# Kernel tuning notes

Hardware: AMD Instinct MI355X
Metric: run time of the kernel (lower is better)

The kernel has to match this reference:

```python
import jax, jax.numpy as jnp
import numpy as np

BS, D = 8192, 1024


def setup_inputs() -> dict:
    key = jax.random.key(0)
    k1, k2, k3, k4 = jax.random.split(key, 4)
    return {
        "z": jax.random.normal(k1, (BS, D), dtype=jnp.float32),
        "w": jax.random.normal(k2, (BS, D), dtype=jnp.float32),
        "u": jax.random.normal(k3, (BS, D), dtype=jnp.float32),
        "b": jax.random.normal(k4, (BS,), dtype=jnp.float32),
    }


def reference(z, w, u, b):
    # --- get_batch_corrected_u ---
    wu = jnp.sum(w * u, axis=1)                      # [bs]
    m = -1.0 + jax.nn.softplus(wu)                   # [bs]
    # NOTE: original divides by sqrt of GLOBAL sum over all of w (no axis)
    w_norm = jnp.sqrt(jnp.sum(w ** 2))               # scalar
    u_hat = u + ((m - wu)[:, None] * w) / w_norm     # [bs, d]

    # --- forward transform: diag(tanh(wTz+b)) @ u  ==  tanh(...)[:,None]*u ---
    inner = jnp.sum(w * z, axis=1) + b               # [bs]
    z_new = z + jnp.tanh(inner)[:, None] * u_hat     # [bs, d]

    # --- det_jcb evaluated with UPDATED z (as in the original code) ---
    inner2 = jnp.sum(w * z_new, axis=1) + b          # [bs]
    h_prime = 1.0 - jnp.tanh(inner2) ** 2            # [bs]
    psi_dot_u = h_prime * jnp.sum(u_hat * w, axis=1) # [bs]
    log_det = jnp.log(jnp.abs(1.0 + psi_dot_u))      # [bs]
    return z_new, log_det
```

## Files before the change

kernel.cpp:

```cpp
#include <hip/hip_runtime.h>
#include <math.h>

#define BS   8192
#define D    1024
#define TPB  256
#define NBLK 512
#define RPB  16
#define RPWV 4
#define F4R  4

typedef float floatx4 __attribute__((ext_vector_type(4)));
typedef unsigned long long u64;

__global__ __launch_bounds__(TPB, 2) void planar_persistent(
    const float* __restrict__ z, const float* __restrict__ w,
    const float* __restrict__ u, const float* __restrict__ b,
    float* __restrict__ zout, float* __restrict__ ldout,
    u64* __restrict__ slots, unsigned int* __restrict__ epoch)
{
    const int t    = threadIdx.x;
    const int wv   = t >> 6;
    const int l    = t & 63;
    const int row0 = blockIdx.x * RPB + wv * RPWV;

    __shared__ unsigned int s_e;
    __shared__ float sw[4], sg[4];
    if (t == 0)
        s_e = __hip_atomic_load(epoch, __ATOMIC_RELAXED,
                                __HIP_MEMORY_SCOPE_AGENT);

    float4 wr[RPWV][F4R];
    float  w2_s[RPWV];
    float  w2acc = 0.f;
#pragma unroll
    for (int r = 0; r < RPWV; ++r) {
        const float4* w4 = (const float4*)w + (size_t)(row0 + r) * (D / 4);
        float w2 = 0.f;
#pragma unroll
        for (int k = 0; k < F4R; ++k) {
            const float4 a = w4[l + (k << 6)];
            wr[r][k] = a;
            w2 += a.x*a.x + a.y*a.y + a.z*a.z + a.w*a.w;
        }
#pragma unroll
        for (int off = 32; off > 0; off >>= 1) w2 += __shfl_xor(w2, off, 64);
        w2_s[r] = w2;
        w2acc  += w2;
    }
    if (l == 0) sw[wv] = w2acc;
    __syncthreads();
    const unsigned int e1 = s_e + 1u;
    if (t == 0) {
        const float p = sw[0] + sw[1] + sw[2] + sw[3];
        const u64 word = ((u64)e1 << 32) | (u64)__float_as_uint(p);
        __hip_atomic_store(&slots[blockIdx.x], word, __ATOMIC_RELAXED,
                           __HIP_MEMORY_SCOPE_AGENT);
    }

    float4 vr[RPWV][F4R];
    float  wu_s[RPWV], in_s[RPWV], th_s[RPWV];
#pragma unroll
    for (int r = 0; r < RPWV; ++r) {
        const int row = row0 + r;
        const float4* z4 = (const float4*)z + (size_t)row * (D / 4);
        const float4* u4 = (const float4*)u + (size_t)row * (D / 4);
        float4 zv[F4R], uv[F4R];
#pragma unroll
        for (int k = 0; k < F4R; ++k) {
            zv[k] = z4[l + (k << 6)];
            uv[k] = u4[l + (k << 6)];
        }
        float wu = 0.f, wz = 0.f;
#pragma unroll
        for (int k = 0; k < F4R; ++k) {
            const float4 a = wr[r][k];
            wu += a.x*uv[k].x + a.y*uv[k].y + a.z*uv[k].z + a.w*uv[k].w;
            wz += a.x*zv[k].x + a.y*zv[k].y + a.z*zv[k].z + a.w*zv[k].w;
        }
#pragma unroll
        for (int off = 32; off > 0; off >>= 1) {
            wu += __shfl_xor(wu, off, 64);
            wz += __shfl_xor(wz, off, 64);
        }
        const float inner = wz + b[row];
        const float tnh   = tanhf(inner);
#pragma unroll
        for (int k = 0; k < F4R; ++k) {
            vr[r][k].x = fmaf(tnh, uv[k].x, zv[k].x);
            vr[r][k].y = fmaf(tnh, uv[k].y, zv[k].y);
            vr[r][k].z = fmaf(tnh, uv[k].z, zv[k].z);
            vr[r][k].w = fmaf(tnh, uv[k].w, zv[k].w);
        }
        wu_s[r] = wu; in_s[r] = inner; th_s[r] = tnh;
    }

    u64 a0, a1;
    for (;;) {
        a0 = __hip_atomic_load(&slots[t], __ATOMIC_RELAXED,
                               __HIP_MEMORY_SCOPE_AGENT);
        a1 = __hip_atomic_load(&slots[t + TPB], __ATOMIC_RELAXED,
                               __HIP_MEMORY_SCOPE_AGENT);
        if ((unsigned int)(a0 >> 32) == e1 &&
            (unsigned int)(a1 >> 32) == e1) break;
        __builtin_amdgcn_s_sleep(4);
    }
    float gs = __uint_as_float((unsigned int)a0)
             + __uint_as_float((unsigned int)a1);
#pragma unroll
    for (int off = 32; off > 0; off >>= 1) gs += __shfl_xor(gs, off, 64);
    if (l == 0) sg[wv] = gs;
    __syncthreads();
    const float wnrm = sqrtf(sg[0] + sg[1] + sg[2] + sg[3]);

    if (blockIdx.x == 0 && t == 0)
        __hip_atomic_store(epoch, e1, __ATOMIC_RELEASE,
                           __HIP_MEMORY_SCOPE_AGENT);

#pragma unroll
    for (int r = 0; r < RPWV; ++r) {
        const int   row  = row0 + r;
        const float wu   = wu_s[r];
        const float sp   = (wu > 0.f) ? (wu + log1pf(expf(-wu)))
                                      : log1pf(expf(wu));
        const float coef = (-1.f + sp - wu) / wnrm;
        const float tc   = th_s[r] * coef;
        floatx4* o4 = (floatx4*)zout + (size_t)row * (D / 4);
#pragma unroll
        for (int k = 0; k < F4R; ++k) {
            floatx4 o;
            o.x = fmaf(tc, wr[r][k].x, vr[r][k].x);
            o.y = fmaf(tc, wr[r][k].y, vr[r][k].y);
            o.z = fmaf(tc, wr[r][k].z, vr[r][k].z);
            o.w = fmaf(tc, wr[r][k].w, vr[r][k].w);
            __builtin_nontemporal_store(o, o4 + l + (k << 6));
        }
        if (l == 0) {
            const float s      = fmaf(coef, w2_s[r], wu);
            const float inner2 = fmaf(th_s[r], s, in_s[r]);
            const float th2    = tanhf(inner2);
            const float hp     = 1.f - th2 * th2;
            ldout[row] = logf(fabsf(fmaf(hp, s, 1.f)));
        }
    }
}

extern "C" void kernel_launch(void* const* d_in, const int* in_sizes, int n_in,
                              void* d_out, int out_size, void* d_ws, size_t ws_size,
                              hipStream_t stream) {
    const float* z = (const float*)d_in[0];
    const float* w = (const float*)d_in[1];
    const float* u = (const float*)d_in[2];
    const float* b = (const float*)d_in[3];

    float* out   = (float*)d_out;
    float* zout  = out;
    float* ldout = out + (size_t)BS * D;

    u64*          slots = (u64*)d_ws;
    unsigned int* epoch = (unsigned int*)(slots + NBLK);

    planar_persistent<<<NBLK, TPB, 0, stream>>>(z, w, u, b, zout, ldout,
                                                slots, epoch);
}
```

Baseline: 24.93 us.

## Split rows into halves, deferring z/u loads for second half past grid barrier

Before the grid-wide spin barrier, only the first two rows per wave load z and u. Loads for the other two rows are issued after the barrier, so their memory traffic overlaps with the output stores of the first half. Register pressure drops because the z+tanh*u intermediates for all four rows no longer have to be held. Each wave now polls all slots itself with __all, which removes the shared-memory reduction and the second __syncthreads. The epoch read and the b loads are hoisted. The cost is more redundant slot polling per wave and some memory latency exposed after the barrier.

Result: slower. 25.86 us (+3.7%).

```diff
diff --git a/kernel.cpp b/kernel.cpp
--- a/kernel.cpp
+++ b/kernel.cpp
@@ -8,6 +8,7 @@
 #define RPB  16
 #define RPWV 4
 #define F4R  4
+#define SPT  (NBLK / 64)
 
 typedef float floatx4 __attribute__((ext_vector_type(4)));
 typedef unsigned long long u64;
@@ -23,11 +24,9 @@
     const int l    = t & 63;
     const int row0 = blockIdx.x * RPB + wv * RPWV;
 
-    __shared__ unsigned int s_e;
-    __shared__ float sw[4], sg[4];
-    if (t == 0)
-        s_e = __hip_atomic_load(epoch, __ATOMIC_RELAXED,
-                                __HIP_MEMORY_SCOPE_AGENT);
+    const unsigned int e1 =
+        __hip_atomic_load(epoch, __ATOMIC_RELAXED, __HIP_MEMORY_SCOPE_AGENT)
+        + 1u;
 
     float4 wr[RPWV][F4R];
     float  w2_s[RPWV];
@@ -47,9 +46,13 @@
         w2_s[r] = w2;
         w2acc  += w2;
     }
+    float brow[RPWV];
+#pragma unroll
+    for (int r = 0; r < RPWV; ++r) brow[r] = b[row0 + r];
+
+    __shared__ float sw[4];
     if (l == 0) sw[wv] = w2acc;
     __syncthreads();
-    const unsigned int e1 = s_e + 1u;
     if (t == 0) {
         const float p = sw[0] + sw[1] + sw[2] + sw[3];
         const u64 word = ((u64)e1 << 32) | (u64)__float_as_uint(p);
@@ -57,10 +60,10 @@
                            __HIP_MEMORY_SCOPE_AGENT);
     }
 
-    float4 vr[RPWV][F4R];
-    float  wu_s[RPWV], in_s[RPWV], th_s[RPWV];
-#pragma unroll
-    for (int r = 0; r < RPWV; ++r) {
+    float4 va[2][F4R];
+    float  wuA[2], inA[2], thA[2];
+#pragma unroll
+    for (int r = 0; r < 2; ++r) {
         const int row = row0 + r;
         const float4* z4 = (const float4*)z + (size_t)row * (D / 4);
         const float4* u4 = (const float4*)u + (size_t)row * (D / 4);
@@ -82,61 +85,122 @@
             wu += __shfl_xor(wu, off, 64);
             wz += __shfl_xor(wz, off, 64);
         }
-        const float inner = wz + b[row];
+        const float inner = wz + brow[r];
         const float tnh   = tanhf(inner);
 #pragma unroll
         for (int k = 0; k < F4R; ++k) {
-            vr[r][k].x = fmaf(tnh, uv[k].x, zv[k].x);
-            vr[r][k].y = fmaf(tnh, uv[k].y, zv[k].y);
-            vr[r][k].z = fmaf(tnh, uv[k].z, zv[k].z);
-            vr[r][k].w = fmaf(tnh, uv[k].w, zv[k].w);
-        }
-        wu_s[r] = wu; in_s[r] = inner; th_s[r] = tnh;
-    }
-
-    u64 a0, a1;
+            va[r][k].x = fmaf(tnh, uv[k].x, zv[k].x);
+            va[r][k].y = fmaf(tnh, uv[k].y, zv[k].y);
+            va[r][k].z = fmaf(tnh, uv[k].z, zv[k].z);
+            va[r][k].w = fmaf(tnh, uv[k].w, zv[k].w);
+        }
+        wuA[r] = wu; inA[r] = inner; thA[r] = tnh;
+    }
+
+    u64 a[SPT];
     for (;;) {
-        a0 = __hip_atomic_load(&slots[t], __ATOMIC_RELAXED,
-                               __HIP_MEMORY_SCOPE_AGENT);
-        a1 = __hip_atomic_load(&slots[t + TPB], __ATOMIC_RELAXED,
-                               __HIP_MEMORY_SCOPE_AGENT);
-        if ((unsigned int)(a0 >> 32) == e1 &&
-            (unsigned int)(a1 >> 32) == e1) break;
+        bool ok = true;
+#pragma unroll
+        for (int i = 0; i < SPT; ++i) {
+            a[i] = __hip_atomic_load(&slots[l + (i << 6)], __ATOMIC_RELAXED,
+                                     __HIP_MEMORY_SCOPE_AGENT);
+            ok = ok && ((unsigned int)(a[i] >> 32) == e1);
+        }
+        if (__all(ok)) break;
         __builtin_amdgcn_s_sleep(4);
     }
-    float gs = __uint_as_float((unsigned int)a0)
-             + __uint_as_float((unsigned int)a1);
+    float gs = 0.f;
+#pragma unroll
+    for (int i = 0; i < SPT; ++i) gs += __uint_as_float((unsigned int)a[i]);
 #pragma unroll
     for (int off = 32; off > 0; off >>= 1) gs += __shfl_xor(gs, off, 64);
-    if (l == 0) sg[wv] = gs;
-    __syncthreads();
-    const float wnrm = sqrtf(sg[0] + sg[1] + sg[2] + sg[3]);
+    const float wnrm = sqrtf(gs);
 
     if (blockIdx.x == 0 && t == 0)
         __hip_atomic_store(epoch, e1, __ATOMIC_RELEASE,
                            __HIP_MEMORY_SCOPE_AGENT);
 
-#pragma unroll
-    for (int r = 0; r < RPWV; ++r) {
+    __builtin_amdgcn_sched_barrier(0);
+
+    float4 zB[2][F4R], uB[2][F4R];
+#pragma unroll
+    for (int r = 0; r < 2; ++r) {
+        const int row = row0 + 2 + r;
+        const float4* z4 = (const float4*)z + (size_t)row * (D / 4);
+        const float4* u4 = (const float4*)u + (size_t)row * (D / 4);
+#pragma unroll
+        for (int k = 0; k < F4R; ++k) {
+            zB[r][k] = z4[l + (k << 6)];
+            uB[r][k] = u4[l + (k << 6)];
+        }
+    }
+
+    __builtin_amdgcn_sched_barrier(0);
+
+#pragma unroll
+    for (int r = 0; r < 2; ++r) {
         const int   row  = row0 + r;
-        const float wu   = wu_s[r];
+        const float wu   = wuA[r];
         const float sp   = (wu > 0.f) ? (wu + log1pf(expf(-wu)))
                                       : log1pf(expf(wu));
         const float coef = (-1.f + sp - wu) / wnrm;
-        const float tc   = th_s[r] * coef;
+        const float tc   = thA[r] * coef;
         floatx4* o4 = (floatx4*)zout + (size_t)row * (D / 4);
 #pragma unroll
         for (int k = 0; k < F4R; ++k) {
             floatx4 o;
-            o.x = fmaf(tc, wr[r][k].x, vr[r][k].x);
-            o.y = fmaf(tc, wr[r][k].y, vr[r][k].y);
-            o.z = fmaf(tc, wr[r][k].z, vr[r][k].z);
-            o.w = fmaf(tc, wr[r][k].w, vr[r][k].w);
+            o.x = fmaf(tc, wr[r][k].x, va[r][k].x);
+            o.y = fmaf(tc, wr[r][k].y, va[r][k].y);
+            o.z = fmaf(tc, wr[r][k].z, va[r][k].z);
+            o.w = fmaf(tc, wr[r][k].w, va[r][k].w);
             __builtin_nontemporal_store(o, o4 + l + (k << 6));
         }
         if (l == 0) {
             const float s      = fmaf(coef, w2_s[r], wu);
-            const float inner2 = fmaf(th_s[r], s, in_s[r]);
+            const float inner2 = fmaf(thA[r], s, inA[r]);
+            const float th2    = tanhf(inner2);
+            const float hp     = 1.f - th2 * th2;
+            ldout[row] = logf(fabsf(fmaf(hp, s, 1.f)));
+        }
+    }
+
+#pragma unroll
+    for (int r = 0; r < 2; ++r) {
+        const int rr  = 2 + r;
+        const int row = row0 + rr;
+        float wu = 0.f, wz = 0.f;
+#pragma unroll
+        for (int k = 0; k < F4R; ++k) {
+            const float4 aa = wr[rr][k];
+            wu += aa.x*uB[r][k].x + aa.y*uB[r][k].y
+                + aa.z*uB[r][k].z + aa.w*uB[r][k].w;
+            wz += aa.x*zB[r][k].x + aa.y*zB[r][k].y
+                + aa.z*zB[r][k].z + aa.w*zB[r][k].w;
+        }
+#pragma unroll
+        for (int off = 32; off > 0; off >>= 1) {
+            wu += __shfl_xor(wu, off, 64);
+            wz += __shfl_xor(wz, off, 64);
+        }
+        const float inner = wz + brow[rr];
+        const float tnh   = tanhf(inner);
+        const float sp    = (wu > 0.f) ? (wu + log1pf(expf(-wu)))
+                                       : log1pf(expf(wu));
+        const float coef  = (-1.f + sp - wu) / wnrm;
+        const float tc    = tnh * coef;
+        floatx4* o4 = (floatx4*)zout + (size_t)row * (D / 4);
+#pragma unroll
+        for (int k = 0; k < F4R; ++k) {
+            floatx4 o;
+            o.x = fmaf(tc, wr[rr][k].x, fmaf(tnh, uB[r][k].x, zB[r][k].x));
+            o.y = fmaf(tc, wr[rr][k].y, fmaf(tnh, uB[r][k].y, zB[r][k].y));
+            o.z = fmaf(tc, wr[rr][k].z, fmaf(tnh, uB[r][k].z, zB[r][k].z));
+            o.w = fmaf(tc, wr[rr][k].w, fmaf(tnh, uB[r][k].w, zB[r][k].w));
+            __builtin_nontemporal_store(o, o4 + l + (k << 6));
+        }
+        if (l == 0) {
+            const float s      = fmaf(coef, w2_s[rr], wu);
+            const float inner2 = fmaf(tnh, s, inner);
             const float th2    = tanhf(inner2);
             const float hp     = 1.f - th2 * th2;
             ldout[row] = logf(fabsf(fmaf(hp, s, 1.f)));
```
